# Performance work log

Hardware: AMD Instinct MI355X
Metric: run time of the kernel (lower is better)

Reference implementation:

```python
import jax, jax.numpy as jnp
import numpy as np

N_NODES = 100000
N_EDGES = 3200000
N_GRAPHS = 256
F_IN, HID, OUT = 8, 64, 9


def gcn_conv(x, src, dst, W, b, n_nodes):
    """PyG GCNConv: x' = D^{-1/2}(A+I)D^{-1/2} (x W) + b, self-loops added."""
    h = x @ W  # [N, H] dense transform first (as in PyG)
    loop = jnp.arange(n_nodes, dtype=src.dtype)
    s = jnp.concatenate([src, loop])  # source of each message
    d = jnp.concatenate([dst, loop])  # destination (aggregation index)
    deg = jax.ops.segment_sum(jnp.ones_like(d, dtype=h.dtype), d, num_segments=n_nodes)
    dinv = jnp.where(deg > 0, jax.lax.rsqrt(deg), 0.0)
    norm = dinv[s] * dinv[d]  # [E+N]
    msg = h[s] * norm[:, None]  # gather + scale
    out = jax.ops.segment_sum(msg, d, num_segments=n_nodes)  # scatter-add
    return out + b


def setup_inputs() -> dict:
    key = jax.random.key(0)
    ks = jax.random.split(key, 20)

    def lin(k, fi, fo):
        bound = 1.0 / np.sqrt(fi)
        k1, k2 = jax.random.split(k)
        W = jax.random.uniform(k1, (fi, fo), jnp.float32, -bound, bound)
        b = jax.random.uniform(k2, (fo,), jnp.float32, -bound, bound)
        return W, b

    x = jax.random.normal(ks[0], (N_NODES, F_IN), jnp.float32)
    edge_index = jax.random.randint(ks[1], (2, N_EDGES), 0, N_NODES, jnp.int32)
    batch = jnp.sort(jax.random.randint(ks[2], (N_NODES,), 0, N_GRAPHS, jnp.int32))

    W1, b1 = lin(ks[3], F_IN, HID)
    W2, b2 = lin(ks[4], HID, HID)
    W3, b3 = lin(ks[5], HID, HID)
    Wg, bg = lin(ks[6], HID, HID)
    Wh1, bh1 = lin(ks[7], HID, HID // 2)
    Wh2, bh2 = lin(ks[8], HID // 2, 1)
    Wm1, bm1 = lin(ks[9], HID, HID)
    Wm2, bm2 = lin(ks[10], HID, OUT)
    Wp1, bp1 = lin(ks[11], HID, HID // 2)
    Wp2, bp2 = lin(ks[12], HID // 2, 1)

    return dict(x=x, edge_index=edge_index, batch=batch,
                W1=W1, b1=b1, W2=W2, b2=b2, W3=W3, b3=b3, Wg=Wg, bg=bg,
                Wh1=Wh1, bh1=bh1, Wh2=Wh2, bh2=bh2,
                Wm1=Wm1, bm1=bm1, Wm2=Wm2, bm2=bm2,
                Wp1=Wp1, bp1=bp1, Wp2=Wp2, bp2=bp2)


def reference(x, edge_index, batch,
              W1, b1, W2, b2, W3, b3, Wg, bg,
              Wh1, bh1, Wh2, bh2, Wm1, bm1, Wm2, bm2, Wp1, bp1, Wp2, bp2):
    src, dst = edge_index[0], edge_index[1]
    n = x.shape[0]

    h = jax.nn.relu(gcn_conv(x, src, dst, W1, b1, n))
    h = jax.nn.relu(gcn_conv(h, src, dst, W2, b2, n))
    h = gcn_conv(h, src, dst, W3, b3, n)

    # global_mean_pool over graphs in the batch
    sums = jax.ops.segment_sum(h, batch, num_segments=N_GRAPHS)
    cnts = jax.ops.segment_sum(jnp.ones((n,), h.dtype), batch, num_segments=N_GRAPHS)
    x_global = sums / jnp.maximum(cnts, 1.0)[:, None]
    x_global = jax.nn.relu(x_global @ Wg + bg)

    heuristic = jax.nn.relu(x_global @ Wh1 + bh1) @ Wh2 + bh2  # [B, 1]
    move_logits = jax.nn.relu(h @ Wm1 + bm1) @ Wm2 + bm2       # [N, 9]
    block_priority = jax.nn.relu(h @ Wp1 + bp1) @ Wp2 + bp2    # [N, 1]
    return heuristic, move_logits, block_priority
```

## Files before the change

kernel.cpp:

```cpp
#include <hip/hip_runtime.h>
#include <hip/hip_fp16.h>

#define N_NODES 100000
#define N_EDGES 3200000
#define N_GRAPHS 256
#define HID 64

#define BSHIFT 9
#define NPB 512
#define NBUCK 196
#define PCHUNK 8192
#define NPBLK 391

__global__ __launch_bounds__(256) void k_hist(
        const int* __restrict__ dst, int* __restrict__ hist) {
    __shared__ int h[NBUCK];
    int t = threadIdx.x;
    for (int j = t; j < NBUCK; j += 256) h[j] = 0;
    __syncthreads();
    int base = blockIdx.x * PCHUNK;
    int end = min(base + PCHUNK, N_EDGES);
    for (int i = base + t; i < end; i += 256)
        atomicAdd(&h[dst[i] >> BSHIFT], 1);
    __syncthreads();
    for (int j = t; j < NBUCK; j += 256)
        hist[(size_t)blockIdx.x * NBUCK + j] = h[j];
}

__global__ __launch_bounds__(512) void k_scan_rows(
        int* __restrict__ hist, int* __restrict__ btotal) {
    __shared__ int s[512];
    int b = blockIdx.x, t = threadIdx.x;
    int v = (t < NPBLK) ? hist[(size_t)t * NBUCK + b] : 0;
    s[t] = v;
    __syncthreads();
    for (int off = 1; off < 512; off <<= 1) {
        int add = (t >= off) ? s[t - off] : 0;
        __syncthreads();
        s[t] += add;
        __syncthreads();
    }
    if (t < NPBLK) hist[(size_t)t * NBUCK + b] = s[t] - v;
    if (t == 511) btotal[b] = s[511];
}

__global__ __launch_bounds__(256) void k_scan_base(
        const int* __restrict__ btotal, int* __restrict__ bbase,
        int* __restrict__ rowp_last) {
    __shared__ int s[256];
    int t = threadIdx.x;
    int v = (t < NBUCK) ? btotal[t] : 0;
    s[t] = v;
    __syncthreads();
    for (int off = 1; off < 256; off <<= 1) {
        int add = (t >= off) ? s[t - off] : 0;
        __syncthreads();
        s[t] += add;
        __syncthreads();
    }
    if (t < NBUCK) bbase[t] = s[t] - v;
    if (t == NBUCK - 1) rowp_last[0] = s[t];
}

__global__ __launch_bounds__(256) void k_scatter(
        const int* __restrict__ src, const int* __restrict__ dst,
        const int* __restrict__ hist, const int* __restrict__ bbase,
        unsigned* __restrict__ pairs) {
    __shared__ int cur[NBUCK];
    int t = threadIdx.x;
    for (int j = t; j < NBUCK; j += 256)
        cur[j] = bbase[j] + hist[(size_t)blockIdx.x * NBUCK + j];
    __syncthreads();
    int base = blockIdx.x * PCHUNK;
    int end = min(base + PCHUNK, N_EDGES);
    for (int i = base + t; i < end; i += 256) {
        int d = dst[i], s = src[i];
        int b = d >> BSHIFT;
        int pos = atomicAdd(&cur[b], 1);
        pairs[pos] = (unsigned)s | ((unsigned)(d & (NPB - 1)) << 17);
    }
}

__global__ __launch_bounds__(512) void k_sort(
        const unsigned* __restrict__ pairs, const int* __restrict__ btotal,
        const int* __restrict__ bbase, int* __restrict__ esrc,
        int* __restrict__ rowp, float* __restrict__ dinv) {
    __shared__ int lcnt[NPB];
    __shared__ int lscan[NPB];
    __shared__ int lcur[NPB];
    int b = blockIdx.x, t = threadIdx.x;
    int nb = btotal[b];
    int base = bbase[b];
    lcnt[t] = 0;
    __syncthreads();
    for (int i = t; i < nb; i += 512) atomicAdd(&lcnt[pairs[base + i] >> 17], 1);
    __syncthreads();
    lscan[t] = lcnt[t];
    __syncthreads();
    for (int off = 1; off < NPB; off <<= 1) {
        int add = (t >= off) ? lscan[t - off] : 0;
        __syncthreads();
        lscan[t] += add;
        __syncthreads();
    }
    lcur[t] = lscan[t] - lcnt[t];
    __syncthreads();
    for (int i = t; i < nb; i += 512) {
        unsigned u = pairs[base + i];
        int d = u >> 17;
        int p = atomicAdd(&lcur[d], 1);
        esrc[base + p] = (int)(u & 0x1FFFFu);
    }
    int node = b * NPB + t;
    if (node < N_NODES) {
        rowp[node] = base + lscan[t] - lcnt[t];
        dinv[node] = rsqrtf((float)lcnt[t] + 1.0f);
    }
}

__global__ __launch_bounds__(256) void k_fold(
        const float* __restrict__ W3, const float* __restrict__ b3,
        const float* __restrict__ Wm1, const float* __restrict__ bm1,
        const float* __restrict__ Wp1, const float* __restrict__ bp1,
        const float* __restrict__ Wg, const float* __restrict__ bg,
        float* __restrict__ Wpack, float* __restrict__ bpack,
        float* __restrict__ Wcg, float* __restrict__ bcg) {
    int tid = blockIdx.x * 256 + threadIdx.x;
    if (tid < 6144) {
        int k = tid / 96, c = tid % 96;
        float s = 0.f;
        if (c < 64) {
#pragma unroll 16
            for (int j = 0; j < 64; ++j) s += W3[k * 64 + j] * Wm1[j * 64 + c];
        } else {
            int cc = c - 64;
#pragma unroll 16
            for (int j = 0; j < 64; ++j) s += W3[k * 64 + j] * Wp1[j * 32 + cc];
        }
        Wpack[tid] = s;
    } else if (tid < 10240) {
        int t2 = tid - 6144;
        int k = t2 / 64, c = t2 % 64;
        float s = 0.f;
#pragma unroll 16
        for (int j = 0; j < 64; ++j) s += W3[k * 64 + j] * Wg[j * 64 + c];
        Wcg[t2] = s;
    } else if (tid < 10336) {
        int c = tid - 10240;
        float s;
        if (c < 64) {
            s = bm1[c];
            for (int j = 0; j < 64; ++j) s += b3[j] * Wm1[j * 64 + c];
        } else {
            int cc = c - 64;
            s = bp1[cc];
            for (int j = 0; j < 64; ++j) s += b3[j] * Wp1[j * 32 + cc];
        }
        bpack[c] = s;
    } else if (tid < 10400) {
        int c = tid - 10336;
        float s = bg[c];
        for (int j = 0; j < 64; ++j) s += b3[j] * Wg[j * 64 + c];
        bcg[c] = s;
    }
}

__global__ __launch_bounds__(256) void k_prepack(
        const float* __restrict__ x, const float* __restrict__ dinv,
        __half* __restrict__ xsh) {
    int n = blockIdx.x * 256 + threadIdx.x;
    if (n >= N_NODES) return;
    float dv = dinv[n];
    const float4* xr = (const float4*)(x + (size_t)n * 8);
    float4 a = xr[0], b = xr[1];
    __half2 h0 = __halves2half2(__float2half_rn(a.x * dv), __float2half_rn(a.y * dv));
    __half2 h1 = __halves2half2(__float2half_rn(a.z * dv), __float2half_rn(a.w * dv));
    __half2 h2 = __halves2half2(__float2half_rn(b.x * dv), __float2half_rn(b.y * dv));
    __half2 h3 = __halves2half2(__float2half_rn(b.z * dv), __float2half_rn(b.w * dv));
    __half2* o = (__half2*)(xsh + (size_t)n * 8);
    o[0] = h0; o[1] = h1; o[2] = h2; o[3] = h3;
}

__global__ __launch_bounds__(256) void k_agg8t(
        const __half* __restrict__ xsh, const float* __restrict__ dinv,
        const int* __restrict__ rp, const int* __restrict__ esrc,
        const float* __restrict__ W1, const float* __restrict__ b1,
        __half* __restrict__ Bout) {
    int gid = (blockIdx.x * 256 + threadIdx.x) >> 5;
    int l = threadIdx.x & 31;
    if (gid >= N_NODES) return;
    int beg = rp[gid], end = rp[gid + 1];
    float a[8];
#pragma unroll
    for (int i = 0; i < 8; ++i) a[i] = 0.f;
    for (int e = beg + l; e < end; e += 32) {
        int s = esrc[e];
        uint4 v = *(const uint4*)(xsh + (size_t)s * 8);
        const __half2* h = (const __half2*)&v;
#pragma unroll
        for (int i = 0; i < 4; ++i) {
            float2 f = __half22float2(h[i]);
            a[2 * i] += f.x; a[2 * i + 1] += f.y;
        }
    }
#pragma unroll
    for (int off = 1; off < 32; off <<= 1) {
#pragma unroll
        for (int i = 0; i < 8; ++i) a[i] += __shfl_xor(a[i], off);
    }
    float dvw = dinv[gid];
    uint4 sv = *(const uint4*)(xsh + (size_t)gid * 8);
    const __half2* sh = (const __half2*)&sv;
    float y[8];
#pragma unroll
    for (int i = 0; i < 4; ++i) {
        float2 fs = __half22float2(sh[i]);
        y[2 * i]     = dvw * (a[2 * i] + fs.x);
        y[2 * i + 1] = dvw * (a[2 * i + 1] + fs.y);
    }
    float acc0 = b1[l], acc1 = b1[l + 32];
#pragma unroll
    for (int k = 0; k < 8; ++k) {
        acc0 += y[k] * W1[k * 64 + l];
        acc1 += y[k] * W1[k * 64 + l + 32];
    }
    Bout[(size_t)gid * 64 + l]      = __float2half_rn(fmaxf(acc0, 0.f) * dvw);
    Bout[(size_t)gid * 64 + l + 32] = __float2half_rn(fmaxf(acc1, 0.f) * dvw);
}

__global__ __launch_bounds__(256) void k_agg64h(
        const __half* __restrict__ B, float* __restrict__ Y,
        const float* __restrict__ dinv, const int* __restrict__ rp,
        const int* __restrict__ esrc) {
    int wid = (blockIdx.x * 256 + threadIdx.x) >> 6;
    int lane = threadIdx.x & 63;
    if (wid >= N_NODES) return;
    int beg = rp[wid], end = rp[wid + 1];
    int g = lane >> 3;
    int fl = (lane & 7) << 3;
    float a0[8], a1[8];
#pragma unroll
    for (int i = 0; i < 8; ++i) { a0[i] = 0.f; a1[i] = 0.f; }
    int e = beg + g;
    for (; e + 8 < end; e += 16) {
        int s0 = esrc[e];
        int s1 = esrc[e + 8];
        uint4 v0 = *(const uint4*)(B + (size_t)s0 * 64 + fl);
        uint4 v1 = *(const uint4*)(B + (size_t)s1 * 64 + fl);
        const __half2* h0 = (const __half2*)&v0;
        const __half2* h1 = (const __half2*)&v1;
#pragma unroll
        for (int i = 0; i < 4; ++i) {
            float2 f0 = __half22float2(h0[i]);
            float2 f1 = __half22float2(h1[i]);
            a0[2 * i] += f0.x; a0[2 * i + 1] += f0.y;
            a1[2 * i] += f1.x; a1[2 * i + 1] += f1.y;
        }
    }
    if (e < end) {
        int s0 = esrc[e];
        uint4 v0 = *(const uint4*)(B + (size_t)s0 * 64 + fl);
        const __half2* h0 = (const __half2*)&v0;
#pragma unroll
        for (int i = 0; i < 4; ++i) {
            float2 f0 = __half22float2(h0[i]);
            a0[2 * i] += f0.x; a0[2 * i + 1] += f0.y;
        }
    }
#pragma unroll
    for (int i = 0; i < 8; ++i) a0[i] += a1[i];
#pragma unroll
    for (int off = 8; off <= 32; off <<= 1) {
#pragma unroll
        for (int i = 0; i < 8; ++i) a0[i] += __shfl_xor(a0[i], off);
    }
    if (lane < 8) {
        uint4 sv = *(const uint4*)(B + (size_t)wid * 64 + fl);
        const __half2* sh = (const __half2*)&sv;
        float dv = dinv[wid];
        float r[8];
#pragma unroll
        for (int i = 0; i < 4; ++i) {
            float2 fs = __half22float2(sh[i]);
            r[2 * i]     = dv * (a0[2 * i] + fs.x);
            r[2 * i + 1] = dv * (a0[2 * i + 1] + fs.y);
        }
        float4 w0 = {r[0], r[1], r[2], r[3]};
        float4 w1 = {r[4], r[5], r[6], r[7]};
        float* yo = Y + (size_t)wid * 64 + fl;
        *(float4*)(yo) = w0;
        *(float4*)(yo + 4) = w1;
    }
}

template <int NCOL, int RELU, int SCALE, int PHEAD, int OUTH>
__global__ __launch_bounds__(NCOL * 4) void k_gemm(
        const float* __restrict__ A, const float* __restrict__ W,
        const float* __restrict__ bias, const float* __restrict__ dinv,
        float* __restrict__ out32, __half* __restrict__ out16,
        const float* __restrict__ Wp2, const float* __restrict__ bp2,
        float* __restrict__ out_p,
        const float* __restrict__ Wm2, const float* __restrict__ bm2,
        float* __restrict__ out_m) {
    __shared__ float Al[128 * 64];
    __shared__ float Wl[64 * NCOL];
    __shared__ float pbuf[PHEAD ? 128 * 8 : 4];
    __shared__ float wm2l[PHEAD ? 64 * 9 : 4];
    __shared__ float bm2l[PHEAD ? 9 : 1];
    const int NTHR = NCOL * 4;
    int tid = threadIdx.x;
    int base = blockIdx.x * 128;

    for (int idx = tid; idx < 128 * 16; idx += NTHR) {
        int r = idx >> 4, c4 = idx & 15;
        float4 v = {0.f, 0.f, 0.f, 0.f};
        if (base + r < N_NODES)
            v = *(const float4*)(A + (size_t)(base + r) * 64 + c4 * 4);
        *(float4*)(Al + r * 64 + c4 * 4) = v;
    }
    for (int idx = tid; idx < 64 * (NCOL / 4); idx += NTHR) {
        int r = idx / (NCOL / 4), c4 = idx % (NCOL / 4);
        *(float4*)(Wl + r * NCOL + c4 * 4) = *(const float4*)(W + r * NCOL + c4 * 4);
    }
    if (PHEAD) {
        for (int i = tid; i < 576; i += NTHR) wm2l[i] = Wm2[i];
        if (tid < 9) bm2l[tid] = bm2[tid];
    }
    __syncthreads();

    int tc = tid % (NCOL / 4);
    int tr = tid / (NCOL / 4);

    float acc[8][4];
#pragma unroll
    for (int i = 0; i < 8; ++i)
#pragma unroll
        for (int c = 0; c < 4; ++c) acc[i][c] = 0.f;

    for (int kb = 0; kb < 16; ++kb) {
        float w0[4], w1[4], w2[4], w3[4];
        {
            const float* wp = Wl + (kb * 4) * NCOL + tc * 4;
            float4 a = *(const float4*)(wp);
            float4 b = *(const float4*)(wp + NCOL);
            float4 c = *(const float4*)(wp + 2 * NCOL);
            float4 d = *(const float4*)(wp + 3 * NCOL);
            w0[0] = a.x; w0[1] = a.y; w0[2] = a.z; w0[3] = a.w;
            w1[0] = b.x; w1[1] = b.y; w1[2] = b.z; w1[3] = b.w;
            w2[0] = c.x; w2[1] = c.y; w2[2] = c.z; w2[3] = c.w;
            w3[0] = d.x; w3[1] = d.y; w3[2] = d.z; w3[3] = d.w;
        }
#pragma unroll
        for (int i = 0; i < 8; ++i) {
            float4 af = *(const float4*)(Al + (tr * 8 + i) * 64 + kb * 4);
#pragma unroll
            for (int c = 0; c < 4; ++c)
                acc[i][c] += af.x * w0[c] + af.y * w1[c] + af.z * w2[c] + af.w * w3[c];
        }
    }

    if (PHEAD) __syncthreads();

    float4 bv = *(const float4*)(bias + tc * 4);
    float wp2l[4] = {0.f, 0.f, 0.f, 0.f};
    if (PHEAD && tc >= 16) {
        float4 wv = *(const float4*)(Wp2 + (tc - 16) * 4);
        wp2l[0] = wv.x; wp2l[1] = wv.y; wp2l[2] = wv.z; wp2l[3] = wv.w;
    }
#pragma unroll
    for (int i = 0; i < 8; ++i) {
        int lr = tr * 8 + i;
        int r = base + lr;
        bool ok = r < N_NODES;
        float o0 = acc[i][0] + bv.x, o1 = acc[i][1] + bv.y;
        float o2 = acc[i][2] + bv.z, o3 = acc[i][3] + bv.w;
        if (RELU) {
            o0 = fmaxf(o0, 0.f); o1 = fmaxf(o1, 0.f);
            o2 = fmaxf(o2, 0.f); o3 = fmaxf(o3, 0.f);
        }
        if (SCALE) {
            float dv = ok ? dinv[r] : 0.f;
            o0 *= dv; o1 *= dv; o2 *= dv; o3 *= dv;
        }
        if (PHEAD) {
            if (tc >= 16) {
                pbuf[lr * 8 + (tc - 16)] =
                    o0 * wp2l[0] + o1 * wp2l[1] + o2 * wp2l[2] + o3 * wp2l[3];
            } else {
                float4 st = {o0, o1, o2, o3};
                *(float4*)(Al + lr * 64 + tc * 4) = st;
            }
        } else if (ok) {
            if (OUTH) {
                __half2 h01 = __halves2half2(__float2half_rn(o0), __float2half_rn(o1));
                __half2 h23 = __halves2half2(__float2half_rn(o2), __float2half_rn(o3));
                __half2* dst = (__half2*)(out16 + (size_t)r * 64 + tc * 4);
                dst[0] = h01; dst[1] = h23;
            } else {
                float4 st = {o0, o1, o2, o3};
                *(float4*)(out32 + (size_t)r * 64 + tc * 4) = st;
            }
        }
    }
    if (PHEAD) {
        __syncthreads();
        for (int o = tid; o < 128 * 9; o += NTHR) {
            int rr = o / 9, j = o - rr * 9;
            int node = base + rr;
            if (node < N_NODES) {
                float s = bm2l[j];
#pragma unroll 16
                for (int k = 0; k < 64; ++k) s += Al[rr * 64 + k] * wm2l[k * 9 + j];
                out_m[(size_t)node * 9 + j] = s;
            }
        }
        if (tid < 128) {
            int r = base + tid;
            if (r < N_NODES) {
                float s = 0.f;
#pragma unroll
                for (int j = 0; j < 8; ++j) s += pbuf[tid * 8 + j];
                out_p[r] = s + bp2[0];
            }
        }
    }
}

__global__ __launch_bounds__(256) void k_graphhead(
        const float* __restrict__ A, const int* __restrict__ batch,
        const float* __restrict__ Wcg, const float* __restrict__ bcg,
        const float* __restrict__ Wh1, const float* __restrict__ bh1,
        const float* __restrict__ Wh2, const float* __restrict__ bh2,
        float* __restrict__ out_h) {
    __shared__ float l[256];
    __shared__ float xgp[64];
    __shared__ float xg[64];
    int gph = blockIdx.x;
    int t = threadIdx.x;
    int lo = 0, hi = N_NODES;
    int target = (t & 1) ? gph + 1 : gph;
    while (lo < hi) {
        int mid = (lo + hi) >> 1;
        if (batch[mid] < target) lo = mid + 1; else hi = mid;
    }
    __shared__ int bounds[2];
    if (t < 2) bounds[t] = lo;
    __syncthreads();
    int beg = bounds[0], end = bounds[1];

    int lane = t & 63, grp = t >> 6;
    float acc = 0.f;
    for (int r = beg + grp; r < end; r += 4) acc += A[(size_t)r * 64 + lane];
    l[t] = acc;
    __syncthreads();
    if (t < 64) {
        float s = l[t] + l[t + 64] + l[t + 128] + l[t + 192];
        xgp[t] = s / fmaxf((float)(end - beg), 1.f);
    }
    __syncthreads();
    {
        int c = t & 63, q = t >> 6;
        float p = 0.f;
#pragma unroll
        for (int k = 0; k < 16; ++k)
            p += xgp[q * 16 + k] * Wcg[(q * 16 + k) * 64 + c];
        l[t] = p;
        __syncthreads();
        if (t < 64)
            xg[t] = fmaxf(l[t] + l[t + 64] + l[t + 128] + l[t + 192] + bcg[t], 0.f);
    }
    __syncthreads();
    if (t < 32) {
        float hj = bh1[t];
#pragma unroll 16
        for (int k = 0; k < 64; ++k) hj += xg[k] * Wh1[k * 32 + t];
        float q = fmaxf(hj, 0.f) * Wh2[t];
#pragma unroll
        for (int off = 16; off; off >>= 1) q += __shfl_xor(q, off);
        if (t == 0) out_h[gph] = q + bh2[0];
    }
}


extern "C" void kernel_launch(void* const* d_in, const int* in_sizes, int n_in,
                              void* d_out, int out_size, void* d_ws, size_t ws_size,
                              hipStream_t stream) {
    const float* x    = (const float*)d_in[0];
    const int*   ei   = (const int*)d_in[1];
    const int*   batch= (const int*)d_in[2];
    const float* W1   = (const float*)d_in[3];
    const float* b1   = (const float*)d_in[4];
    const float* W2   = (const float*)d_in[5];
    const float* b2   = (const float*)d_in[6];
    const float* W3   = (const float*)d_in[7];
    const float* b3   = (const float*)d_in[8];
    const float* Wg   = (const float*)d_in[9];
    const float* bg   = (const float*)d_in[10];
    const float* Wh1  = (const float*)d_in[11];
    const float* bh1  = (const float*)d_in[12];
    const float* Wh2  = (const float*)d_in[13];
    const float* bh2  = (const float*)d_in[14];
    const float* Wm1  = (const float*)d_in[15];
    const float* bm1  = (const float*)d_in[16];
    const float* Wm2  = (const float*)d_in[17];
    const float* bm2  = (const float*)d_in[18];
    const float* Wp1  = (const float*)d_in[19];
    const float* bp1  = (const float*)d_in[20];
    const float* Wp2  = (const float*)d_in[21];
    const float* bp2  = (const float*)d_in[22];

    const int* e_src = ei;
    const int* e_dst = ei + N_EDGES;

    char* ws = (char*)d_ws;
    size_t off = 0;
    auto alloc = [&](size_t bytes) {
        void* p = ws + off;
        off += (bytes + 255) & ~(size_t)255;
        return p;
    };
    float* bufA   = (float*)alloc(N_NODES * 64 * sizeof(float));
    float* bufB   = (float*)alloc(N_NODES * 64 * sizeof(float));
    float* dinv   = (float*)alloc(N_NODES * sizeof(float));
    int*   rowp   = (int*)  alloc((N_NODES + 1) * sizeof(int));
    int*   esrc   = (int*)  alloc(N_EDGES * sizeof(int));
    int*   hist   = (int*)  alloc((size_t)NBUCK * NPBLK * sizeof(int));
    int*   btotal = (int*)  alloc(NBUCK * sizeof(int));
    int*   bbase  = (int*)  alloc(NBUCK * sizeof(int));
    __half* xsh   = (__half*)alloc(N_NODES * 8 * sizeof(__half));
    float* Wpack  = (float*)alloc(64 * 96 * sizeof(float));
    float* bpack  = (float*)alloc(96 * sizeof(float));
    float* Wcg    = (float*)alloc(64 * 64 * sizeof(float));
    float* bcg    = (float*)alloc(64 * sizeof(float));
    unsigned* pairs = (unsigned*)bufA;
    __half* B2h = (__half*)bufB;
    __half* B3h = (__half*)(bufB + 3200000);
    (void)ws_size; (void)n_in; (void)in_sizes; (void)out_size;

    float* out_h = (float*)d_out;
    float* out_m = (float*)d_out + 256;
    float* out_p = (float*)d_out + 256 + 900000;

    const int TB = 256;
    dim3 blkWave((N_NODES * 64 + TB - 1) / TB);
    dim3 blkHalf((N_NODES * 32 + TB - 1) / TB);
    const int NT = 782;

    k_hist<<<NPBLK, TB, 0, stream>>>(e_dst, hist);
    k_scan_rows<<<NBUCK, 512, 0, stream>>>(hist, btotal);
    k_scan_base<<<1, 256, 0, stream>>>(btotal, bbase, rowp + N_NODES);
    k_scatter<<<NPBLK, TB, 0, stream>>>(e_src, e_dst, hist, bbase, pairs);
    k_sort<<<NBUCK, 512, 0, stream>>>(pairs, btotal, bbase, esrc, rowp, dinv);

    k_fold<<<41, TB, 0, stream>>>(W3, b3, Wm1, bm1, Wp1, bp1, Wg, bg,
                                  Wpack, bpack, Wcg, bcg);

    k_prepack<<<(N_NODES + TB - 1) / TB, TB, 0, stream>>>(x, dinv, xsh);
    k_agg8t<<<blkHalf, TB, 0, stream>>>(xsh, dinv, rowp, esrc, W1, b1, B2h);
    k_agg64h<<<blkWave, TB, 0, stream>>>(B2h, bufA, dinv, rowp, esrc);
    k_gemm<64, 1, 1, 0, 1><<<NT, 256, 0, stream>>>(
        bufA, W2, b2, dinv, nullptr, B3h,
        nullptr, nullptr, nullptr, nullptr, nullptr, nullptr);
    k_agg64h<<<blkWave, TB, 0, stream>>>(B3h, bufA, dinv, rowp, esrc);

    k_gemm<96, 1, 0, 1, 0><<<NT, 384, 0, stream>>>(
        bufA, Wpack, bpack, nullptr, nullptr, nullptr,
        Wp2, bp2, out_p, Wm2, bm2, out_m);

    k_graphhead<<<N_GRAPHS, TB, 0, stream>>>(bufA, batch, Wcg, bcg,
                                             Wh1, bh1, Wh2, bh2, out_h);
}
```

Measured before the change: 334.0 us.

## Replace tiled head GEMM with per-node register kernel and specialize layer-2 GEMM

The templated shared-memory GEMM is split into a dedicated 64-column kernel for layer 2 (ReLU, dinv scale, fp16 output) and a new per-thread head kernel. In the head kernel each thread holds one node's 64 features in registers and computes the 96 packed hidden units, the 9 move logits and the priority output directly, reading weights through uniform global loads. This drops the shared-memory staging, the extra barriers and the second pass over the move head. The cost is 64+ live registers per thread, which may lower occupancy, and weight reads that depend on cache broadcast.

```diff
diff --git a/kernel.cpp b/kernel.cpp
--- a/kernel.cpp
+++ b/kernel.cpp
@@ -293,43 +293,30 @@
     }
 }
 
-template <int NCOL, int RELU, int SCALE, int PHEAD, int OUTH>
-__global__ __launch_bounds__(NCOL * 4) void k_gemm(
+__global__ __launch_bounds__(256) void k_gemm64(
         const float* __restrict__ A, const float* __restrict__ W,
         const float* __restrict__ bias, const float* __restrict__ dinv,
-        float* __restrict__ out32, __half* __restrict__ out16,
-        const float* __restrict__ Wp2, const float* __restrict__ bp2,
-        float* __restrict__ out_p,
-        const float* __restrict__ Wm2, const float* __restrict__ bm2,
-        float* __restrict__ out_m) {
+        __half* __restrict__ out16) {
     __shared__ float Al[128 * 64];
-    __shared__ float Wl[64 * NCOL];
-    __shared__ float pbuf[PHEAD ? 128 * 8 : 4];
-    __shared__ float wm2l[PHEAD ? 64 * 9 : 4];
-    __shared__ float bm2l[PHEAD ? 9 : 1];
-    const int NTHR = NCOL * 4;
+    __shared__ float Wl[64 * 64];
     int tid = threadIdx.x;
     int base = blockIdx.x * 128;
 
-    for (int idx = tid; idx < 128 * 16; idx += NTHR) {
+    for (int idx = tid; idx < 128 * 16; idx += 256) {
         int r = idx >> 4, c4 = idx & 15;
         float4 v = {0.f, 0.f, 0.f, 0.f};
         if (base + r < N_NODES)
             v = *(const float4*)(A + (size_t)(base + r) * 64 + c4 * 4);
         *(float4*)(Al + r * 64 + c4 * 4) = v;
     }
-    for (int idx = tid; idx < 64 * (NCOL / 4); idx += NTHR) {
-        int r = idx / (NCOL / 4), c4 = idx % (NCOL / 4);
-        *(float4*)(Wl + r * NCOL + c4 * 4) = *(const float4*)(W + r * NCOL + c4 * 4);
-    }
-    if (PHEAD) {
-        for (int i = tid; i < 576; i += NTHR) wm2l[i] = Wm2[i];
-        if (tid < 9) bm2l[tid] = bm2[tid];
-    }
-    __syncthreads();
-
-    int tc = tid % (NCOL / 4);
-    int tr = tid / (NCOL / 4);
+    for (int idx = tid; idx < 64 * 16; idx += 256) {
+        int r = idx >> 4, c4 = idx & 15;
+        *(float4*)(Wl + r * 64 + c4 * 4) = *(const float4*)(W + r * 64 + c4 * 4);
+    }
+    __syncthreads();
+
+    int tc = tid & 15;
+    int tr = tid >> 4;
 
     float acc[8][4];
 #pragma unroll
@@ -340,11 +327,11 @@
     for (int kb = 0; kb < 16; ++kb) {
         float w0[4], w1[4], w2[4], w3[4];
         {
-            const float* wp = Wl + (kb * 4) * NCOL + tc * 4;
+            const float* wp = Wl + (kb * 4) * 64 + tc * 4;
             float4 a = *(const float4*)(wp);
-            float4 b = *(const float4*)(wp + NCOL);
-            float4 c = *(const float4*)(wp + 2 * NCOL);
-            float4 d = *(const float4*)(wp + 3 * NCOL);
+            float4 b = *(const float4*)(wp + 64);
+            float4 c = *(const float4*)(wp + 128);
+            float4 d = *(const float4*)(wp + 192);
             w0[0] = a.x; w0[1] = a.y; w0[2] = a.z; w0[3] = a.w;
             w1[0] = b.x; w1[1] = b.y; w1[2] = b.z; w1[3] = b.w;
             w2[0] = c.x; w2[1] = c.y; w2[2] = c.z; w2[3] = c.w;
@@ -359,71 +346,60 @@
         }
     }
 
-    if (PHEAD) __syncthreads();
-
     float4 bv = *(const float4*)(bias + tc * 4);
-    float wp2l[4] = {0.f, 0.f, 0.f, 0.f};
-    if (PHEAD && tc >= 16) {
-        float4 wv = *(const float4*)(Wp2 + (tc - 16) * 4);
-        wp2l[0] = wv.x; wp2l[1] = wv.y; wp2l[2] = wv.z; wp2l[3] = wv.w;
-    }
 #pragma unroll
     for (int i = 0; i < 8; ++i) {
-        int lr = tr * 8 + i;
-        int r = base + lr;
-        bool ok = r < N_NODES;
-        float o0 = acc[i][0] + bv.x, o1 = acc[i][1] + bv.y;
-        float o2 = acc[i][2] + bv.z, o3 = acc[i][3] + bv.w;
-        if (RELU) {
-            o0 = fmaxf(o0, 0.f); o1 = fmaxf(o1, 0.f);
-            o2 = fmaxf(o2, 0.f); o3 = fmaxf(o3, 0.f);
-        }
-        if (SCALE) {
-            float dv = ok ? dinv[r] : 0.f;
-            o0 *= dv; o1 *= dv; o2 *= dv; o3 *= dv;
-        }
-        if (PHEAD) {
-            if (tc >= 16) {
-                pbuf[lr * 8 + (tc - 16)] =
-                    o0 * wp2l[0] + o1 * wp2l[1] + o2 * wp2l[2] + o3 * wp2l[3];
-            } else {
-                float4 st = {o0, o1, o2, o3};
-                *(float4*)(Al + lr * 64 + tc * 4) = st;
-            }
-        } else if (ok) {
-            if (OUTH) {
-                __half2 h01 = __halves2half2(__float2half_rn(o0), __float2half_rn(o1));
-                __half2 h23 = __halves2half2(__float2half_rn(o2), __float2half_rn(o3));
-                __half2* dst = (__half2*)(out16 + (size_t)r * 64 + tc * 4);
-                dst[0] = h01; dst[1] = h23;
-            } else {
-                float4 st = {o0, o1, o2, o3};
-                *(float4*)(out32 + (size_t)r * 64 + tc * 4) = st;
-            }
-        }
-    }
-    if (PHEAD) {
-        __syncthreads();
-        for (int o = tid; o < 128 * 9; o += NTHR) {
-            int rr = o / 9, j = o - rr * 9;
-            int node = base + rr;
-            if (node < N_NODES) {
-                float s = bm2l[j];
+        int r = base + tr * 8 + i;
+        if (r < N_NODES) {
+            float dv = dinv[r];
+            float o0 = fmaxf(acc[i][0] + bv.x, 0.f) * dv;
+            float o1 = fmaxf(acc[i][1] + bv.y, 0.f) * dv;
+            float o2 = fmaxf(acc[i][2] + bv.z, 0.f) * dv;
+            float o3 = fmaxf(acc[i][3] + bv.w, 0.f) * dv;
+            __half2 h01 = __halves2half2(__float2half_rn(o0), __float2half_rn(o1));
+            __half2 h23 = __halves2half2(__float2half_rn(o2), __float2half_rn(o3));
+            __half2* dst = (__half2*)(out16 + (size_t)r * 64 + tc * 4);
+            dst[0] = h01; dst[1] = h23;
+        }
+    }
+}
+
+__global__ __launch_bounds__(256) void k_headreg(
+        const float* __restrict__ Y, const float* __restrict__ Wpack,
+        const float* __restrict__ bpack,
+        const float* __restrict__ Wm2, const float* __restrict__ bm2,
+        const float* __restrict__ Wp2, const float* __restrict__ bp2,
+        float* __restrict__ out_m, float* __restrict__ out_p) {
+    int n = blockIdx.x * 256 + threadIdx.x;
+    if (n >= N_NODES) return;
+    float y[64];
+    const float4* yr = (const float4*)(Y + (size_t)n * 64);
+#pragma unroll
+    for (int i = 0; i < 16; ++i) {
+        float4 v = yr[i];
+        y[4 * i] = v.x; y[4 * i + 1] = v.y; y[4 * i + 2] = v.z; y[4 * i + 3] = v.w;
+    }
+    float om[9];
+#pragma unroll
+    for (int j = 0; j < 9; ++j) om[j] = bm2[j];
+    for (int f = 0; f < 64; ++f) {
+        float m = bpack[f];
 #pragma unroll 16
-                for (int k = 0; k < 64; ++k) s += Al[rr * 64 + k] * wm2l[k * 9 + j];
-                out_m[(size_t)node * 9 + j] = s;
-            }
-        }
-        if (tid < 128) {
-            int r = base + tid;
-            if (r < N_NODES) {
-                float s = 0.f;
-#pragma unroll
-                for (int j = 0; j < 8; ++j) s += pbuf[tid * 8 + j];
-                out_p[r] = s + bp2[0];
-            }
-        }
-    }
+        for (int k = 0; k < 64; ++k) m += y[k] * Wpack[k * 96 + f];
+        m = fmaxf(m, 0.f);
+#pragma unroll
+        for (int j = 0; j < 9; ++j) om[j] += m * Wm2[f * 9 + j];
+    }
+    float op = bp2[0];
+    for (int f = 0; f < 32; ++f) {
+        float p = bpack[64 + f];
+#pragma unroll 16
+        for (int k = 0; k < 64; ++k) p += y[k] * Wpack[k * 96 + 64 + f];
+        op += fmaxf(p, 0.f) * Wp2[f];
+    }
+#pragma unroll
+    for (int j = 0; j < 9; ++j) out_m[(size_t)n * 9 + j] = om[j];
+    out_p[n] = op;
 }
 
 __global__ __launch_bounds__(256) void k_graphhead(
@@ -558,14 +534,11 @@
     k_prepack<<<(N_NODES + TB - 1) / TB, TB, 0, stream>>>(x, dinv, xsh);
     k_agg8t<<<blkHalf, TB, 0, stream>>>(xsh, dinv, rowp, esrc, W1, b1, B2h);
     k_agg64h<<<blkWave, TB, 0, stream>>>(B2h, bufA, dinv, rowp, esrc);
-    k_gemm<64, 1, 1, 0, 1><<<NT, 256, 0, stream>>>(
-        bufA, W2, b2, dinv, nullptr, B3h,
-        nullptr, nullptr, nullptr, nullptr, nullptr, nullptr);
+    k_gemm64<<<NT, 256, 0, stream>>>(bufA, W2, b2, dinv, B3h);
     k_agg64h<<<blkWave, TB, 0, stream>>>(B3h, bufA, dinv, rowp, esrc);
 
-    k_gemm<96, 1, 0, 1, 0><<<NT, 384, 0, stream>>>(
-        bufA, Wpack, bpack, nullptr, nullptr, nullptr,
-        Wp2, bp2, out_p, Wm2, bm2, out_m);
+    k_headreg<<<(N_NODES + TB - 1) / TB, TB, 0, stream>>>(
+        bufA, Wpack, bpack, Wm2, bm2, Wp2, bp2, out_m, out_p);
 
     k_graphhead<<<N_GRAPHS, TB, 0, stream>>>(bufA, batch, Wcg, bcg,
                                              Wh1, bh1, Wh2, bh2, out_h);
```

New measurement: 619.5 us. 1.85x slower.
